# Performance work log

Hardware: AMD Instinct MI355X
Metric: run time of the kernel (lower is better)

## Reference

```python
import jax, jax.numpy as jnp
import numpy as np
from jax import lax

D_MODEL = 1024
N_HEADS = 16
D_STATE = 1024
D_INNER = 1024
D_CONV = 4
CHUNK = 64
BATCH = 2
SEQ = 4096
CONV_DIM = 2 * D_STATE + D_INNER  # 3072
D_IN_PROJ = CONV_DIM + N_HEADS    # 3088


def segsum(a):
    """a: [..., T] -> [..., T, T] segment-sum: out[i,j] = sum_{j<k<=i} a[k], -inf above diag."""
    T = a.shape[-1]
    idx = jnp.arange(T)
    strict = idx[:, None] > idx[None, :]          # i > j
    xx = jnp.where(strict, a[..., :, None], 0.0)  # broadcast a along new last (e) dim
    s = jnp.cumsum(xx, axis=-2)
    incl = idx[:, None] >= idx[None, :]
    return jnp.where(incl, s, -jnp.inf)


def ssd(xv, A, Bm, Cm, l):
    """Mamba-2 SSD chunked scan with max-normalized decays and norm denominator.
    xv:[b,S,h,p] A:[b,S,h] Bm:[b,S,h,n] Cm:[b,S,h,n]"""
    b, S, h, p = xv.shape
    n = Bm.shape[-1]
    c = S // l
    xv = xv.reshape(b, c, l, h, p)
    A = A.reshape(b, c, l, h)
    Bm = Bm.reshape(b, c, l, h, n)
    Cm = Cm.reshape(b, c, l, h, n)
    A = jnp.transpose(A, (0, 3, 1, 2))                  # b h c l
    A_cumsum = jnp.cumsum(A, axis=-1)                   # b h c l
    L_log = segsum(A)                                   # b h c l l
    L = jnp.exp(L_log - jnp.max(L_log, axis=-1, keepdims=True))
    norm_diag = jnp.transpose(L.sum(-1), (0, 2, 3, 1))  # b c l h
    Y_diag = jnp.einsum('bclhn,bcshn,bhcls,bcshp->bclhp', Cm, Bm, L, xv)
    decay_states = A_cumsum[..., -1:] - A_cumsum        # b h c l
    decay_states = jnp.exp(decay_states - jnp.max(decay_states, axis=-1, keepdims=True))
    norm_decay = jnp.transpose(decay_states.sum(-1), (0, 2, 1))  # b c h
    states = jnp.einsum('bclhn,bhcl,bclhp->bchpn', Bm, decay_states, xv)
    norm_decay = jnp.pad(norm_decay, ((0, 0), (1, 0), (0, 0)))
    states = jnp.pad(states, ((0, 0), (1, 0), (0, 0), (0, 0), (0, 0)))
    A_last = jnp.pad(A_cumsum[..., -1], ((0, 0), (0, 0), (1, 0)))  # b h c+1
    decay_chunk = segsum(A_last)                        # b h c+1 c+1
    decay_chunk = jnp.exp(decay_chunk - jnp.max(decay_chunk, axis=-1, keepdims=True))
    norm_decay = jnp.einsum('bhzc,bch->bzh', decay_chunk, norm_decay)[:, :-1]  # b c h
    states = jnp.einsum('bhzc,bchpn->bzhpn', decay_chunk, states)[:, :-1]      # b c h p n
    state_decay_out = jnp.exp(A_cumsum - jnp.max(A_cumsum, axis=-1, keepdims=True))
    norm_off = jnp.einsum('bch,bhcl->bclh', norm_decay, state_decay_out)
    Y_off = jnp.einsum('bclhn,bchpn,bhcl->bclhp', Cm, states, state_decay_out)
    Y = (Y_diag + Y_off).reshape(b, S, h, p)
    norm = (norm_diag + norm_off).reshape(b, S, h)
    return Y / norm[..., None]


def setup_inputs() -> dict:
    key = jax.random.key(0)
    ks = jax.random.split(key, 6)
    x = jax.random.normal(ks[0], (BATCH, SEQ, D_MODEL), dtype=jnp.float32)
    in_proj_w = jax.random.normal(ks[1], (D_IN_PROJ, D_MODEL), dtype=jnp.float32) * 0.02
    conv_w = jax.random.normal(ks[2], (CONV_DIM, 1, D_CONV), dtype=jnp.float32) * 0.3
    conv_b = jnp.zeros((CONV_DIM,), dtype=jnp.float32)
    w_base = jax.random.uniform(ks[3], (N_HEADS,), dtype=jnp.float32, minval=-0.5, maxval=0.5)
    out_proj_w = jax.random.normal(ks[4], (D_MODEL, D_INNER), dtype=jnp.float32) * 0.02
    return {"x": x, "in_proj_w": in_proj_w, "conv_w": conv_w, "conv_b": conv_b,
            "w_base": w_base, "out_proj_w": out_proj_w}


def reference(x, in_proj_w, conv_w, conv_b, w_base, out_proj_w):
    b, S, _ = x.shape  # S divisible by CHUNK -> no padding branch
    xIOw = x @ in_proj_w.T                                  # [b,S,3088]
    xIO, w = xIOw[..., :CONV_DIM], xIOw[..., CONV_DIM:]
    # causal depthwise conv1d (pad d_conv-1 on both sides, keep first S == left pad)
    y = lax.conv_general_dilated(
        jnp.transpose(xIO, (0, 2, 1)), conv_w, window_strides=(1,),
        padding=[(D_CONV - 1, 0)], feature_group_count=CONV_DIM,
        dimension_numbers=('NCH', 'OIH', 'NCH'))
    xIO = jnp.transpose(y + conv_b[None, :, None], (0, 2, 1))  # [b,S,3072]
    xs = xIO[..., :D_STATE].reshape(b, S, N_HEADS, D_STATE // N_HEADS)
    I = xIO[..., D_STATE:2 * D_STATE].reshape(b, S, N_HEADS, D_STATE // N_HEADS)
    O = xIO[..., 2 * D_STATE:].reshape(b, S, N_HEADS, D_INNER // N_HEADS)
    w = w * w_base                                          # [b,S,h]
    out = ssd(O, w, I, xs, CHUNK)                           # [b,S,h,p]
    out = out.reshape(b, S, D_INNER) @ out_proj_w.T
    return out[:, :S]
```

## Files before the change

kernel.cpp:

```cpp
#include <hip/hip_runtime.h>
#include <hip/hip_bf16.h>
#include <math.h>
#include <stdint.h>

#define SEQL 4096
#define NH 16
#define CDIM 3072
#define DPROJ 3088
#define DMODEL 1024

typedef __hip_bfloat16 bf16;
typedef __bf16 nbf16;
typedef __attribute__((ext_vector_type(8))) __bf16 bf16x8;
typedef __attribute__((ext_vector_type(4))) float f32x4;

__device__ inline void store_val(float* p, float v) { *p = v; }
__device__ inline void store_val(nbf16* p, float v) { *p = (nbf16)v; }

__device__ __forceinline__ void gload_lds16(const void* g, void* l) {
  __builtin_amdgcn_global_load_lds(
      (const __attribute__((address_space(1))) void*)g,
      (__attribute__((address_space(3))) void*)l, 16, 0, 0);
}

__device__ __forceinline__ int swz(int row, int col) {
  return row * 64 + (col ^ ((row & 7) << 3));
}

template <typename TOUT>
__global__ __launch_bounds__(256) void gemm_mfma(const nbf16* __restrict__ A,
                                                 const nbf16* __restrict__ B,
                                                 TOUT* __restrict__ C,
                                                 int M, int N, int K) {
  __shared__ __align__(16) nbf16 Alds[128 * 64];
  __shared__ __align__(16) nbf16 Blds[128 * 64];
  int tid = threadIdx.x;
  int lane = tid & 63;
  int w = tid >> 6, wm = w >> 1, wn = w & 1;
  int bm = blockIdx.y * 128, bn = blockIdx.x * 128;
  f32x4 acc[4][4] = {};
  const nbf16* Ag = A + (size_t)bm * K;
  const nbf16* Bg = B + (size_t)bn * K;
  for (int k0 = 0; k0 < K; k0 += 64) {
#pragma unroll
    for (int q = 0; q < 4; ++q) {
      int e = (q * 256 + tid) * 8;
      int row = e >> 6, col = e & 63;
      gload_lds16(Ag + (size_t)row * K + k0 + col, &Alds[e]);
      gload_lds16(Bg + (size_t)row * K + k0 + col, &Blds[e]);
    }
    __syncthreads();
#pragma unroll
    for (int kk = 0; kk < 64; kk += 32) {
      bf16x8 af[4], bfr[4];
#pragma unroll
      for (int i = 0; i < 4; ++i) {
        af[i]  = *(const bf16x8*)&Alds[(wm * 64 + i * 16 + (lane & 15)) * 64 + kk + (lane >> 4) * 8];
        bfr[i] = *(const bf16x8*)&Blds[(wn * 64 + i * 16 + (lane & 15)) * 64 + kk + (lane >> 4) * 8];
      }
#pragma unroll
      for (int mi = 0; mi < 4; ++mi)
#pragma unroll
        for (int ni = 0; ni < 4; ++ni)
          acc[mi][ni] = __builtin_amdgcn_mfma_f32_16x16x32_bf16(af[mi], bfr[ni], acc[mi][ni], 0, 0, 0);
    }
    __syncthreads();
  }
#pragma unroll
  for (int mi = 0; mi < 4; ++mi)
#pragma unroll
    for (int ni = 0; ni < 4; ++ni) {
      int colw = bn + wn * 64 + ni * 16 + (lane & 15);
      if (colw >= N) continue;
#pragma unroll
      for (int j = 0; j < 4; ++j) {
        int roww = bm + wm * 64 + mi * 16 + (lane >> 4) * 4 + j;
        store_val(&C[(size_t)roww * N + colw], acc[mi][ni][j]);
      }
    }
}

__global__ __launch_bounds__(256) void cast_bf16(const float* __restrict__ in,
                                                 nbf16* __restrict__ out, long n) {
  long i = ((long)blockIdx.x * 256 + threadIdx.x) * 4;
  if (i >= n) return;
  float4 v = *(const float4*)(in + i);
  out[i] = (nbf16)v.x; out[i + 1] = (nbf16)v.y;
  out[i + 2] = (nbf16)v.z; out[i + 3] = (nbf16)v.w;
}

__global__ __launch_bounds__(256) void cast_pad_w(const float* __restrict__ in,
                                                  nbf16* __restrict__ out) {
  long i = ((long)blockIdx.x * 256 + threadIdx.x) * 4;
  if (i >= (long)3200 * 1024) return;
  int row = (int)(i >> 10);
  if (row < DPROJ) {
    float4 v = *(const float4*)(in + i);
    out[i] = (nbf16)v.x; out[i + 1] = (nbf16)v.y;
    out[i + 2] = (nbf16)v.z; out[i + 3] = (nbf16)v.w;
  } else {
    out[i] = (nbf16)0.f; out[i + 1] = (nbf16)0.f;
    out[i + 2] = (nbf16)0.f; out[i + 3] = (nbf16)0.f;
  }
}

__global__ __launch_bounds__(256) void ssd_intra(
    const nbf16* __restrict__ xw, const float* __restrict__ cw,
    const float* __restrict__ cb, const float* __restrict__ wbase,
    float* __restrict__ Ybuf, float* __restrict__ states,
    float* __restrict__ norm_diag, float* __restrict__ sdo_g,
    float* __restrict__ ndecay, float* __restrict__ Alast) {
  __shared__ __align__(16) nbf16 Craw[68 * 64];
  __shared__ __align__(16) nbf16 Braw[68 * 64];
  __shared__ __align__(16) nbf16 Xraw[68 * 64];
  __shared__ __align__(16) nbf16 BbT[64 * 64];
  __shared__ __align__(16) nbf16 XbT[64 * 64];
  __shared__ float cums_s[64], mincs_s[64], dec_s[64];
  nbf16* Sb = Xraw;

  int tid = threadIdx.x;
  int lane = tid & 63;
  int w = tid >> 6;
  int h = blockIdx.x & 15;
  int c = (blockIdx.x >> 4) & 63;
  int b = blockIdx.x >> 10;

  for (int i = tid; i < 67 * 64; i += 256) {
    int row = i >> 6, n = i & 63;
    int t = c * 64 - 3 + row;
    nbf16 vc = (nbf16)0.f, vb = vc, vx = vc;
    if (t >= 0) {
      const nbf16* r = xw + ((size_t)(b * SEQL + t)) * DPROJ + h * 64 + n;
      vc = r[0]; vb = r[1024]; vx = r[2048];
    }
    int idx = swz(row, n);
    Craw[idx] = vc; Braw[idx] = vb; Xraw[idx] = vx;
  }

  if (w == 0) {
    float a = (float)xw[((size_t)(b * SEQL + c * 64 + lane)) * DPROJ + CDIM + h] * wbase[h];
    float cum = a;
#pragma unroll
    for (int d = 1; d < 64; d <<= 1) {
      float t = __shfl_up(cum, d, 64);
      if (lane >= d) cum += t;
    }
    float mn = cum;
#pragma unroll
    for (int d = 1; d < 64; d <<= 1) {
      float t = __shfl_up(mn, d, 64);
      if (lane >= d) mn = fminf(mn, t);
    }
    float mnall = __shfl(mn, 63, 64);
    float mx = cum;
#pragma unroll
    for (int d = 1; d < 64; d <<= 1) mx = fmaxf(mx, __shfl_xor(mx, d, 64));
    float dec = expf(mnall - cum);
    float sdo = expf(cum - mx);
    float nd = dec;
#pragma unroll
    for (int d = 1; d < 64; d <<= 1) nd += __shfl_xor(nd, d, 64);
    cums_s[lane] = cum; mincs_s[lane] = mn; dec_s[lane] = dec;
    sdo_g[(size_t)blockIdx.x * 64 + lane] = sdo;
    if (lane == 0) ndecay[blockIdx.x] = nd;
    if (lane == 63) Alast[((size_t)(b * NH + h)) * 64 + c] = cum;
  }
  __syncthreads();

  float rc[16], rb[16], rx[16];
  {
    int n = tid & 63, base = tid >> 6;
    const float* wcc = cw + (size_t)(h * 64 + n) * 4;
    const float* wcb = wcc + 4096;
    const float* wcx = wcc + 8192;
    float bcc = cb[h * 64 + n], bcb = cb[1024 + h * 64 + n], bcx = cb[2048 + h * 64 + n];
#pragma unroll
    for (int q = 0; q < 16; ++q) {
      int l = base + q * 4;
      float aC = bcc, aB = bcb, aX = bcx;
#pragma unroll
      for (int d = 0; d < 4; ++d) {
        int idx = swz(l + d, n);
        aC = fmaf((float)Craw[idx], wcc[d], aC);
        aB = fmaf((float)Braw[idx], wcb[d], aB);
        aX = fmaf((float)Xraw[idx], wcx[d], aX);
      }
      rc[q] = aC; rb[q] = aB; rx[q] = aX;
    }
  }
  __syncthreads();
  {
    int n = tid & 63, base = tid >> 6;
#pragma unroll
    for (int q = 0; q < 16; ++q) {
      int l = base + q * 4;
      Craw[swz(l, n)] = (nbf16)rc[q];
      Braw[swz(l, n)] = (nbf16)rb[q];
      BbT[swz(n, l)] = (nbf16)rb[q];
      XbT[swz(n, l)] = (nbf16)rx[q];
    }
  }
  __syncthreads();

  {
    f32x4 accS[4] = {};
#pragma unroll
    for (int kk = 0; kk < 64; kk += 32) {
      int arow = w * 16 + (lane & 15);
      int c0 = kk + (lane >> 4) * 8;
      bf16x8 af = *(const bf16x8*)&Craw[swz(arow, c0)];
#pragma unroll
      for (int nb = 0; nb < 4; ++nb) {
        int brow = nb * 16 + (lane & 15);
        bf16x8 bfr = *(const bf16x8*)&Braw[swz(brow, c0)];
        accS[nb] = __builtin_amdgcn_mfma_f32_16x16x32_bf16(af, bfr, accS[nb], 0, 0, 0);
      }
    }
    float rowsum[4] = {0.f, 0.f, 0.f, 0.f};
#pragma unroll
    for (int nb = 0; nb < 4; ++nb) {
      int s = nb * 16 + (lane & 15);
      float cs = cums_s[s];
#pragma unroll
      for (int r = 0; r < 4; ++r) {
        int l = w * 16 + (lane >> 4) * 4 + r;
        float e = (s <= l) ? expf(mincs_s[l] - cs) : 0.f;
        rowsum[r] += e;
        Sb[swz(l, s)] = (nbf16)(accS[nb][r] * e);
      }
    }
#pragma unroll
    for (int r = 0; r < 4; ++r) {
#pragma unroll
      for (int d = 1; d < 16; d <<= 1) rowsum[r] += __shfl_xor(rowsum[r], d, 64);
      if ((lane & 15) == 0) {
        int l = w * 16 + (lane >> 4) * 4 + r;
        norm_diag[(size_t)blockIdx.x * 64 + l] = rowsum[r];
      }
    }
  }
  __syncthreads();

  {
    f32x4 accY[4] = {};
#pragma unroll
    for (int kk = 0; kk < 64; kk += 32) {
      int arow = w * 16 + (lane & 15);
      int c0 = kk + (lane >> 4) * 8;
      bf16x8 af = *(const bf16x8*)&Sb[swz(arow, c0)];
#pragma unroll
      for (int pb = 0; pb < 4; ++pb) {
        int prow = pb * 16 + (lane & 15);
        bf16x8 bfr = *(const bf16x8*)&XbT[swz(prow, c0)];
        accY[pb] = __builtin_amdgcn_mfma_f32_16x16x32_bf16(af, bfr, accY[pb], 0, 0, 0);
      }
    }
    size_t ybase = ((size_t)(b * SEQL + c * 64)) * DMODEL + h * 64;
#pragma unroll
    for (int pb = 0; pb < 4; ++pb) {
      int p = pb * 16 + (lane & 15);
#pragma unroll
      for (int r = 0; r < 4; ++r) {
        int l = w * 16 + (lane >> 4) * 4 + r;
        Ybuf[ybase + (size_t)l * DMODEL + p] = accY[pb][r];
      }
    }
  }

  {
    f32x4 accT[4] = {};
#pragma unroll
    for (int kk = 0; kk < 64; kk += 32) {
      int prow = w * 16 + (lane & 15);
      int c0 = kk + (lane >> 4) * 8;
      bf16x8 xf = *(const bf16x8*)&XbT[swz(prow, c0)];
      bf16x8 af;
#pragma unroll
      for (int j = 0; j < 8; ++j) af[j] = (nbf16)((float)xf[j] * dec_s[c0 + j]);
#pragma unroll
      for (int nb = 0; nb < 4; ++nb) {
        int nrow = nb * 16 + (lane & 15);
        bf16x8 bfr = *(const bf16x8*)&BbT[swz(nrow, c0)];
        accT[nb] = __builtin_amdgcn_mfma_f32_16x16x32_bf16(af, bfr, accT[nb], 0, 0, 0);
      }
    }
    size_t sbase = (size_t)blockIdx.x * 4096;
#pragma unroll
    for (int nb = 0; nb < 4; ++nb) {
      int n = nb * 16 + (lane & 15);
#pragma unroll
      for (int r = 0; r < 4; ++r) {
        int p = w * 16 + (lane >> 4) * 4 + r;
        states[sbase + p * 64 + n] = accT[nb][r];
      }
    }
  }
}

__global__ __launch_bounds__(256) void ssd_scan(
    const float* __restrict__ Alast, float* __restrict__ states,
    const float* __restrict__ ndecay, float* __restrict__ nd_in) {
  __shared__ float cA[64], cB[64];
  int tid = threadIdx.x;
  int pg = blockIdx.x & 15, h = (blockIdx.x >> 4) & 15, b = blockIdx.x >> 8;
  if (tid == 0) {
    float cum = 0.f, minc = 0.f, ndR = 0.f;
    if (pg == 0) nd_in[(b * 64 + 0) * 16 + h] = 0.f;
    for (int z = 1; z < 64; ++z) {
      cum += Alast[(b * NH + h) * 64 + (z - 1)];
      float nm = fminf(minc, cum);
      cA[z] = expf(nm - minc);
      cB[z] = expf(nm - cum);
      minc = nm;
      ndR = cA[z] * ndR + cB[z] * ndecay[(b * 64 + (z - 1)) * 16 + h];
      if (pg == 0) nd_in[(b * 64 + z) * 16 + h] = ndR;
    }
  }
  __syncthreads();
  int off = pg * 256 + tid;
  float R = 0.f;
  for (int z = 1; z < 64; ++z) {
    size_t slot = ((size_t)(b * 64 + (z - 1)) * 16 + h) * 4096 + off;
    R = cA[z] * R + cB[z] * states[slot];
    states[slot] = R;
  }
}

__global__ __launch_bounds__(256) void ssd_off(
    const nbf16* __restrict__ xw, const float* __restrict__ cw,
    const float* __restrict__ cb, const float* __restrict__ states,
    const float* __restrict__ norm_diag, const float* __restrict__ sdo_g,
    const float* __restrict__ nd_in, const float* __restrict__ Ybuf,
    nbf16* __restrict__ Ybf) {
  __shared__ __align__(16) nbf16 Craw[68 * 64];
  __shared__ __align__(16) nbf16 Ssb[64 * 64];
  int tid = threadIdx.x, lane = tid & 63, w = tid >> 6;
  int h = blockIdx.x & 15, c = (blockIdx.x >> 4) & 63, b = blockIdx.x >> 10;

  for (int i = tid; i < 67 * 64; i += 256) {
    int row = i >> 6, n = i & 63;
    int t = c * 64 - 3 + row;
    nbf16 v = (nbf16)0.f;
    if (t >= 0) v = xw[((size_t)(b * SEQL + t)) * DPROJ + h * 64 + n];
    Craw[swz(row, n)] = v;
  }
  if (c > 0) {
    size_t sbase = (((size_t)(b * 64 + (c - 1)) * 16 + h)) * 4096;
    for (int i = tid; i < 4096; i += 256) {
      int p = i >> 6, n = i & 63;
      Ssb[swz(p, n)] = (nbf16)states[sbase + i];
    }
  } else {
    for (int i = tid; i < 4096; i += 256) Ssb[i] = (nbf16)0.f;
  }
  __syncthreads();

  float rc[16];
  {
    int n = tid & 63, base = tid >> 6;
    const float* wcc = cw + (size_t)(h * 64 + n) * 4;
    float bcc = cb[h * 64 + n];
#pragma unroll
    for (int q = 0; q < 16; ++q) {
      int l = base + q * 4;
      float aC = bcc;
#pragma unroll
      for (int d = 0; d < 4; ++d) aC = fmaf((float)Craw[swz(l + d, n)], wcc[d], aC);
      rc[q] = aC;
    }
  }
  __syncthreads();
  {
    int n = tid & 63, base = tid >> 6;
#pragma unroll
    for (int q = 0; q < 16; ++q) Craw[swz(base + q * 4, n)] = (nbf16)rc[q];
  }
  __syncthreads();

  f32x4 accO[4] = {};
#pragma unroll
  for (int kk = 0; kk < 64; kk += 32) {
    int arow = w * 16 + (lane & 15);
    int c0 = kk + (lane >> 4) * 8;
    bf16x8 af = *(const bf16x8*)&Craw[swz(arow, c0)];
#pragma unroll
    for (int pb = 0; pb < 4; ++pb) {
      int prow = pb * 16 + (lane & 15);
      bf16x8 bfr = *(const bf16x8*)&Ssb[swz(prow, c0)];
      accO[pb] = __builtin_amdgcn_mfma_f32_16x16x32_bf16(af, bfr, accO[pb], 0, 0, 0);
    }
  }
  float ndin = nd_in[blockIdx.x];
  size_t ybase = ((size_t)(b * SEQL + c * 64)) * DMODEL + h * 64;
#pragma unroll
  for (int r = 0; r < 4; ++r) {
    int l = w * 16 + (lane >> 4) * 4 + r;
    float sd = sdo_g[(size_t)blockIdx.x * 64 + l];
    float nrm = norm_diag[(size_t)blockIdx.x * 64 + l] + ndin * sd;
#pragma unroll
    for (int pb = 0; pb < 4; ++pb) {
      int p = pb * 16 + (lane & 15);
      size_t yi = ybase + (size_t)l * DMODEL + p;
      Ybf[yi] = (nbf16)((Ybuf[yi] + accO[pb][r] * sd) / nrm);
    }
  }
}

extern "C" void kernel_launch(void* const* d_in, const int* in_sizes, int n_in,
                              void* d_out, int out_size, void* d_ws, size_t ws_size,
                              hipStream_t stream) {
  const float* x          = (const float*)d_in[0];
  const float* in_proj_w  = (const float*)d_in[1];
  const float* conv_w     = (const float*)d_in[2];
  const float* conv_b     = (const float*)d_in[3];
  const float* w_base     = (const float*)d_in[4];
  const float* out_proj_w = (const float*)d_in[5];
  float* out = (float*)d_out;

  char* ws = (char*)d_ws;
  size_t off = 0;
  auto alloc = [&](size_t bytes) {
    void* p = ws + off;
    off += (bytes + 255) & ~(size_t)255;
    return p;
  };
  const size_t BT = (size_t)2 * SEQL;
  nbf16* xIOw = (nbf16*)alloc(BT * DPROJ * 2);
  float* Ybuf = (float*)alloc(BT * DMODEL * 4);
  nbf16* xbf  = (nbf16*)alloc(BT * DMODEL * 2);
  nbf16* wibf = (nbf16*)alloc((size_t)3200 * 1024 * 2);
  nbf16* wobf = (nbf16*)alloc((size_t)1024 * 1024 * 2);
  float* norm_diag = (float*)alloc((size_t)2048 * 64 * 4);
  float* sdo   = (float*)alloc((size_t)2048 * 64 * 4);
  float* ndec  = (float*)alloc((size_t)2048 * 4);
  float* Alast = (float*)alloc((size_t)2048 * 4);
  float* nd_in = (float*)alloc((size_t)2048 * 4);
  nbf16* Ybf = xbf;
  float* states = out;

  cast_bf16<<<(int)(BT * DMODEL / 4 / 256), 256, 0, stream>>>(x, xbf, BT * DMODEL);
  cast_pad_w<<<3200 * 1024 / 4 / 256, 256, 0, stream>>>(in_proj_w, wibf);
  cast_bf16<<<DMODEL * DMODEL / 4 / 256, 256, 0, stream>>>(out_proj_w, wobf, (long)DMODEL * DMODEL);
  gemm_mfma<nbf16><<<dim3(25, BT / 128), 256, 0, stream>>>(
      xbf, wibf, xIOw, (int)BT, DPROJ, DMODEL);
  ssd_intra<<<2048, 256, 0, stream>>>(xIOw, conv_w, conv_b, w_base,
                                      Ybuf, states, norm_diag, sdo, ndec, Alast);
  ssd_scan<<<512, 256, 0, stream>>>(Alast, states, ndec, nd_in);
  ssd_off<<<2048, 256, 0, stream>>>(xIOw, conv_w, conv_b, states,
                                    norm_diag, sdo, nd_in, Ybuf, Ybf);
  gemm_mfma<float><<<dim3(DMODEL / 128, BT / 128), 256, 0, stream>>>(
      Ybf, wobf, out, (int)BT, DMODEL, DMODEL);
}
```

Measured before the change: 336.0 us.

## Recast inter-chunk scan as MFMA matmul, shrink intermediates to bf16, retile GEMMs

The serial per-chunk state recurrence in ssd_scan is replaced by a dense lower-triangular decay matrix multiplied against all chunk states with MFMA, so the states are no longer read and written chunk by chunk. Intra-chunk outputs and states are now stored in bf16 instead of fp32, which cuts workspace traffic, and the Y buffer is updated in place. The GEMMs move to 256x128 tiles with 512 threads and a swizzled workgroup order for cache locality, and the LDS staging loads are vectorised to 8 elements. The cost is extra bf16 rounding on states and partial outputs, plus more LDS per GEMM block.

```diff
diff --git a/kernel.cpp b/kernel.cpp
--- a/kernel.cpp
+++ b/kernel.cpp
@@ -9,7 +9,6 @@
 #define DPROJ 3088
 #define DMODEL 1024
 
-typedef __hip_bfloat16 bf16;
 typedef __bf16 nbf16;
 typedef __attribute__((ext_vector_type(8))) __bf16 bf16x8;
 typedef __attribute__((ext_vector_type(4))) float f32x4;
@@ -28,25 +27,34 @@
 }
 
 template <typename TOUT>
-__global__ __launch_bounds__(256) void gemm_mfma(const nbf16* __restrict__ A,
+__global__ __launch_bounds__(512) void gemm_mfma(const nbf16* __restrict__ A,
                                                  const nbf16* __restrict__ B,
                                                  TOUT* __restrict__ C,
                                                  int M, int N, int K) {
-  __shared__ __align__(16) nbf16 Alds[128 * 64];
+  __shared__ __align__(16) nbf16 Alds[256 * 64];
   __shared__ __align__(16) nbf16 Blds[128 * 64];
   int tid = threadIdx.x;
   int lane = tid & 63;
   int w = tid >> 6, wm = w >> 1, wn = w & 1;
-  int bm = blockIdx.y * 128, bn = blockIdx.x * 128;
+  int gx = gridDim.x;
+  int nwg = gx * gridDim.y;
+  int orig = blockIdx.y * gx + blockIdx.x;
+  int wg = (orig & 7) * (nwg >> 3) + (orig >> 3);
+  int bm = (wg / gx) * 256, bn = (wg % gx) * 128;
   f32x4 acc[4][4] = {};
   const nbf16* Ag = A + (size_t)bm * K;
   const nbf16* Bg = B + (size_t)bn * K;
   for (int k0 = 0; k0 < K; k0 += 64) {
 #pragma unroll
     for (int q = 0; q < 4; ++q) {
-      int e = (q * 256 + tid) * 8;
+      int e = (q * 512 + tid) * 8;
       int row = e >> 6, col = e & 63;
       gload_lds16(Ag + (size_t)row * K + k0 + col, &Alds[e]);
+    }
+#pragma unroll
+    for (int q = 0; q < 2; ++q) {
+      int e = (q * 512 + tid) * 8;
+      int row = e >> 6, col = e & 63;
       gload_lds16(Bg + (size_t)row * K + k0 + col, &Blds[e]);
     }
     __syncthreads();
@@ -107,7 +115,7 @@
 __global__ __launch_bounds__(256) void ssd_intra(
     const nbf16* __restrict__ xw, const float* __restrict__ cw,
     const float* __restrict__ cb, const float* __restrict__ wbase,
-    float* __restrict__ Ybuf, float* __restrict__ states,
+    nbf16* __restrict__ Ydg, nbf16* __restrict__ stG,
     float* __restrict__ norm_diag, float* __restrict__ sdo_g,
     float* __restrict__ ndecay, float* __restrict__ Alast) {
   __shared__ __align__(16) nbf16 Craw[68 * 64];
@@ -125,16 +133,20 @@
   int c = (blockIdx.x >> 4) & 63;
   int b = blockIdx.x >> 10;
 
-  for (int i = tid; i < 67 * 64; i += 256) {
-    int row = i >> 6, n = i & 63;
+  for (int i = tid; i < 67 * 8; i += 256) {
+    int row = i >> 3, n0 = (i & 7) * 8;
     int t = c * 64 - 3 + row;
-    nbf16 vc = (nbf16)0.f, vb = vc, vx = vc;
+    bf16x8 vc = {}, vb = {}, vx = {};
     if (t >= 0) {
-      const nbf16* r = xw + ((size_t)(b * SEQL + t)) * DPROJ + h * 64 + n;
-      vc = r[0]; vb = r[1024]; vx = r[2048];
-    }
-    int idx = swz(row, n);
-    Craw[idx] = vc; Braw[idx] = vb; Xraw[idx] = vx;
+      const nbf16* r = xw + ((size_t)(b * SEQL + t)) * DPROJ + h * 64 + n0;
+      vc = *(const bf16x8*)(r);
+      vb = *(const bf16x8*)(r + 1024);
+      vx = *(const bf16x8*)(r + 2048);
+    }
+    int idx = swz(row, n0);
+    *(bf16x8*)&Craw[idx] = vc;
+    *(bf16x8*)&Braw[idx] = vb;
+    *(bf16x8*)&Xraw[idx] = vx;
   }
 
   if (w == 0) {
@@ -262,7 +274,7 @@
 #pragma unroll
       for (int r = 0; r < 4; ++r) {
         int l = w * 16 + (lane >> 4) * 4 + r;
-        Ybuf[ybase + (size_t)l * DMODEL + p] = accY[pb][r];
+        Ydg[ybase + (size_t)l * DMODEL + p] = (nbf16)accY[pb][r];
       }
     }
   }
@@ -284,74 +296,130 @@
         accT[nb] = __builtin_amdgcn_mfma_f32_16x16x32_bf16(af, bfr, accT[nb], 0, 0, 0);
       }
     }
-    size_t sbase = (size_t)blockIdx.x * 4096;
+    size_t sbase = (((size_t)(b * NH + h)) * 64 + c) * 4096;
 #pragma unroll
     for (int nb = 0; nb < 4; ++nb) {
       int n = nb * 16 + (lane & 15);
 #pragma unroll
       for (int r = 0; r < 4; ++r) {
         int p = w * 16 + (lane >> 4) * 4 + r;
-        states[sbase + p * 64 + n] = accT[nb][r];
+        stG[sbase + p * 64 + n] = (nbf16)accT[nb][r];
       }
     }
   }
 }
 
 __global__ __launch_bounds__(256) void ssd_scan(
-    const float* __restrict__ Alast, float* __restrict__ states,
-    const float* __restrict__ ndecay, float* __restrict__ nd_in) {
-  __shared__ float cA[64], cB[64];
-  int tid = threadIdx.x;
-  int pg = blockIdx.x & 15, h = (blockIdx.x >> 4) & 15, b = blockIdx.x >> 8;
-  if (tid == 0) {
-    float cum = 0.f, minc = 0.f, ndR = 0.f;
-    if (pg == 0) nd_in[(b * 64 + 0) * 16 + h] = 0.f;
-    for (int z = 1; z < 64; ++z) {
-      cum += Alast[(b * NH + h) * 64 + (z - 1)];
-      float nm = fminf(minc, cum);
-      cA[z] = expf(nm - minc);
-      cB[z] = expf(nm - cum);
-      minc = nm;
-      ndR = cA[z] * ndR + cB[z] * ndecay[(b * 64 + (z - 1)) * 16 + h];
-      if (pg == 0) nd_in[(b * 64 + z) * 16 + h] = ndR;
-    }
-  }
-  __syncthreads();
-  int off = pg * 256 + tid;
-  float R = 0.f;
-  for (int z = 1; z < 64; ++z) {
-    size_t slot = ((size_t)(b * 64 + (z - 1)) * 16 + h) * 4096 + off;
-    R = cA[z] * R + cB[z] * states[slot];
-    states[slot] = R;
-  }
+    const float* __restrict__ Alast, const nbf16* __restrict__ stG,
+    const float* __restrict__ ndecay, nbf16* __restrict__ siG,
+    float* __restrict__ nd_in) {
+  __shared__ __align__(16) nbf16 Msw[64 * 64];
+  __shared__ __align__(16) nbf16 StT[256 * 64];
+  __shared__ float Qs[66], mzS[64];
+  int tid = threadIdx.x, lane = tid & 63, w = tid >> 6;
+  int et = blockIdx.x & 15, h = (blockIdx.x >> 4) & 15, b = blockIdx.x >> 8;
+
+  if (w == 0) {
+    float a = Alast[((size_t)(b * NH + h)) * 64 + lane];
+    float s = a;
+#pragma unroll
+    for (int d = 1; d < 64; d <<= 1) {
+      float t = __shfl_up(s, d, 64);
+      if (lane >= d) s += t;
+    }
+    float Q = __shfl_up(s, 1, 64);
+    if (lane == 0) Q = 0.f;
+    float m = Q;
+#pragma unroll
+    for (int d = 1; d < 64; d <<= 1) {
+      float t = __shfl_up(m, d, 64);
+      if (lane >= d) m = fminf(m, t);
+    }
+    Qs[lane] = Q; mzS[lane] = m;
+    if (lane == 0) { Qs[64] = 0.f; Qs[65] = 0.f; }
+  }
+  __syncthreads();
+
+#pragma unroll
+  for (int k = 0; k < 16; ++k) {
+    int i = tid + (k << 8);
+    int z = i >> 6, j = i & 63;
+    float v = (j < z) ? expf(mzS[z] - Qs[j + 1]) : 0.f;
+    Msw[swz(z, j)] = (nbf16)v;
+  }
+  size_t stbase = ((size_t)(b * NH + h)) * 64 * 4096 + et * 256;
+#pragma unroll
+  for (int q = 0; q < 8; ++q) {
+    int i = tid + (q << 8);
+    int cc = i >> 5, oct = i & 31;
+    bf16x8 v = *(const bf16x8*)&stG[stbase + (size_t)cc * 4096 + oct * 8];
+#pragma unroll
+    for (int jj = 0; jj < 8; ++jj) StT[swz(oct * 8 + jj, cc)] = v[jj];
+  }
+  __syncthreads();
+
+  if (et == 0 && tid < 64) {
+    int z = tid;
+    float acc = 0.f;
+    for (int j = 0; j < z; ++j)
+      acc += expf(mzS[z] - Qs[j + 1]) * ndecay[((size_t)(b * 64 + j)) * 16 + h];
+    nd_in[((size_t)(b * 64 + z)) * 16 + h] = acc;
+  }
+
+  f32x4 acc[4][4] = {};
+#pragma unroll
+  for (int kk = 0; kk < 64; kk += 32) {
+    int c0 = kk + (lane >> 4) * 8;
+    bf16x8 af[4], bfr[4];
+#pragma unroll
+    for (int i = 0; i < 4; ++i) {
+      af[i]  = *(const bf16x8*)&Msw[swz(i * 16 + (lane & 15), c0)];
+      bfr[i] = *(const bf16x8*)&StT[swz(w * 64 + i * 16 + (lane & 15), c0)];
+    }
+#pragma unroll
+    for (int mi = 0; mi < 4; ++mi)
+#pragma unroll
+      for (int ni = 0; ni < 4; ++ni)
+        acc[mi][ni] = __builtin_amdgcn_mfma_f32_16x16x32_bf16(af[mi], bfr[ni], acc[mi][ni], 0, 0, 0);
+  }
+  size_t obase = ((size_t)(b * NH + h)) * 64 * 4096 + et * 256;
+#pragma unroll
+  for (int mi = 0; mi < 4; ++mi)
+#pragma unroll
+    for (int ni = 0; ni < 4; ++ni) {
+      int e = w * 64 + ni * 16 + (lane & 15);
+#pragma unroll
+      for (int r = 0; r < 4; ++r) {
+        int z = mi * 16 + (lane >> 4) * 4 + r;
+        siG[obase + (size_t)z * 4096 + e] = (nbf16)acc[mi][ni][r];
+      }
+    }
 }
 
 __global__ __launch_bounds__(256) void ssd_off(
     const nbf16* __restrict__ xw, const float* __restrict__ cw,
-    const float* __restrict__ cb, const float* __restrict__ states,
+    const float* __restrict__ cb, const nbf16* __restrict__ siG,
     const float* __restrict__ norm_diag, const float* __restrict__ sdo_g,
-    const float* __restrict__ nd_in, const float* __restrict__ Ybuf,
-    nbf16* __restrict__ Ybf) {
+    const float* __restrict__ nd_in, nbf16* __restrict__ Ydg) {
   __shared__ __align__(16) nbf16 Craw[68 * 64];
   __shared__ __align__(16) nbf16 Ssb[64 * 64];
   int tid = threadIdx.x, lane = tid & 63, w = tid >> 6;
   int h = blockIdx.x & 15, c = (blockIdx.x >> 4) & 63, b = blockIdx.x >> 10;
 
-  for (int i = tid; i < 67 * 64; i += 256) {
-    int row = i >> 6, n = i & 63;
+  for (int i = tid; i < 67 * 8; i += 256) {
+    int row = i >> 3, n0 = (i & 7) * 8;
     int t = c * 64 - 3 + row;
-    nbf16 v = (nbf16)0.f;
-    if (t >= 0) v = xw[((size_t)(b * SEQL + t)) * DPROJ + h * 64 + n];
-    Craw[swz(row, n)] = v;
-  }
-  if (c > 0) {
-    size_t sbase = (((size_t)(b * 64 + (c - 1)) * 16 + h)) * 4096;
-    for (int i = tid; i < 4096; i += 256) {
-      int p = i >> 6, n = i & 63;
-      Ssb[swz(p, n)] = (nbf16)states[sbase + i];
-    }
-  } else {
-    for (int i = tid; i < 4096; i += 256) Ssb[i] = (nbf16)0.f;
+    bf16x8 v = {};
+    if (t >= 0) v = *(const bf16x8*)(xw + ((size_t)(b * SEQL + t)) * DPROJ + h * 64 + n0);
+    *(bf16x8*)&Craw[swz(row, n0)] = v;
+  }
+  {
+    size_t sbase = (((size_t)(b * NH + h)) * 64 + c) * 4096;
+    for (int i = tid; i < 512; i += 256) {
+      int p = i >> 3, n0 = (i & 7) * 8;
+      bf16x8 v = *(const bf16x8*)&siG[sbase + p * 64 + n0];
+      *(bf16x8*)&Ssb[swz(p, n0)] = v;
+    }
   }
   __syncthreads();
 
@@ -401,7 +469,7 @@
     for (int pb = 0; pb < 4; ++pb) {
       int p = pb * 16 + (lane & 15);
       size_t yi = ybase + (size_t)l * DMODEL + p;
-      Ybf[yi] = (nbf16)((Ybuf[yi] + accO[pb][r] * sd) / nrm);
+      Ydg[yi] = (nbf16)(((float)Ydg[yi] + accO[pb][r] * sd) / nrm);
     }
   }
 }
@@ -426,28 +494,28 @@
   };
   const size_t BT = (size_t)2 * SEQL;
   nbf16* xIOw = (nbf16*)alloc(BT * DPROJ * 2);
-  float* Ybuf = (float*)alloc(BT * DMODEL * 4);
   nbf16* xbf  = (nbf16*)alloc(BT * DMODEL * 2);
   nbf16* wibf = (nbf16*)alloc((size_t)3200 * 1024 * 2);
   nbf16* wobf = (nbf16*)alloc((size_t)1024 * 1024 * 2);
+  nbf16* stG  = (nbf16*)alloc((size_t)2048 * 4096 * 2);
+  nbf16* siG  = (nbf16*)alloc((size_t)2048 * 4096 * 2);
   float* norm_diag = (float*)alloc((size_t)2048 * 64 * 4);
   float* sdo   = (float*)alloc((size_t)2048 * 64 * 4);
   float* ndec  = (float*)alloc((size_t)2048 * 4);
   float* Alast = (float*)alloc((size_t)2048 * 4);
   float* nd_in = (float*)alloc((size_t)2048 * 4);
-  nbf16* Ybf = xbf;
-  float* states = out;
+  nbf16* Ydg = xbf;
 
   cast_bf16<<<(int)(BT * DMODEL / 4 / 256), 256, 0, stream>>>(x, xbf, BT * DMODEL);
   cast_pad_w<<<3200 * 1024 / 4 / 256, 256, 0, stream>>>(in_proj_w, wibf);
   cast_bf16<<<DMODEL * DMODEL / 4 / 256, 256, 0, stream>>>(out_proj_w, wobf, (long)DMODEL * DMODEL);
-  gemm_mfma<nbf16><<<dim3(25, BT / 128), 256, 0, stream>>>(
+  gemm_mfma<nbf16><<<dim3(25, BT / 256), 512, 0, stream>>>(
       xbf, wibf, xIOw, (int)BT, DPROJ, DMODEL);
   ssd_intra<<<2048, 256, 0, stream>>>(xIOw, conv_w, conv_b, w_base,
-                                      Ybuf, states, norm_diag, sdo, ndec, Alast);
-  ssd_scan<<<512, 256, 0, stream>>>(Alast, states, ndec, nd_in);
-  ssd_off<<<2048, 256, 0, stream>>>(xIOw, conv_w, conv_b, states,
-                                    norm_diag, sdo, nd_in, Ybuf, Ybf);
-  gemm_mfma<float><<<dim3(DMODEL / 128, BT / 128), 256, 0, stream>>>(
-      Ybf, wobf, out, (int)BT, DMODEL, DMODEL);
-}
+                                      Ydg, stG, norm_diag, sdo, ndec, Alast);
+  ssd_scan<<<512, 256, 0, stream>>>(Alast, stG, ndec, siG, nd_in);
+  ssd_off<<<2048, 256, 0, stream>>>(xIOw, conv_w, conv_b, siG,
+                                    norm_diag, sdo, nd_in, Ydg);
+  gemm_mfma<float><<<dim3(DMODEL / 128, BT / 256), 512, 0, stream>>>(
+      Ydg, wobf, out, (int)BT, DMODEL, DMODEL);
+}
```

After: 301.9 us. 1.11x faster.
